# Performance work log

Hardware: AMD Instinct MI355X
Metric: run time of the kernel (lower is better)

Reference implementation:

```python
import jax, jax.numpy as jnp
import numpy as np

B, L, D = 16, 2048, 128
GROUP = 16
NG = L // GROUP  # number of groups per batch
ALPHA = 0.5


def setup_inputs() -> dict:
    key = jax.random.key(0)
    k0, k1, k2 = jax.random.split(key, 3)
    x = jax.random.normal(k0, (B, L, D), dtype=jnp.float32)
    # per-batch permutation = gather indices (each position used exactly once)
    group_tensor = jax.vmap(lambda k: jax.random.permutation(k, L))(
        jax.random.split(k1, B)).astype(jnp.int32)
    ctxlens = jnp.full((B,), L, dtype=jnp.int32)
    W = jax.random.normal(k2, (2 * D,), dtype=jnp.float32) * (1.0 / np.sqrt(D))
    norm_alpha = jnp.ones((2,), dtype=jnp.float32)
    norm_gamma = jnp.ones((2 * D,), dtype=jnp.float32)
    norm_beta = jnp.zeros((2 * D,), dtype=jnp.float32)
    return {"x": x, "group_tensor": group_tensor, "ctxlens": ctxlens, "W": W,
            "norm_alpha": norm_alpha, "norm_gamma": norm_gamma, "norm_beta": norm_beta}


def _leaky_relu(v):
    return jnp.where(v >= 0, v, 0.01 * v)


def _ncn_forward(x, group_tensor, ctxlens, W, norm_alpha, norm_gamma, norm_beta):
    Bd, Ld, Dd = x.shape
    ng = Ld // GROUP
    Wi, Wj = W[:Dd], W[Dd:]
    a1, a2 = norm_alpha[0], norm_alpha[1]
    g1, g2 = norm_gamma[:Dd], norm_gamma[Dd:]
    b1, b2 = norm_beta[:Dd], norm_beta[Dd:]

    # gather x by group indices -> [B, NG, GROUP, D]
    xg = jnp.take_along_axis(x, group_tensor[:, :, None].astype(jnp.int32), axis=1)
    xg = xg.reshape(Bd, ng, GROUP, Dd)

    def step(carry, j):
        xi, xa = carry  # each [B, NG, GROUP, D]
        xj = jax.lax.dynamic_slice_in_dim(xi, j, 1, axis=2)  # [B, NG, 1, D]
        sim = jnp.einsum('bgnd,d->bgn', xi, Wi) \
            + jnp.einsum('bgd,d->bg', xj[:, :, 0, :], Wj)[:, :, None]  # [B,NG,GROUP]
        T = ALPHA * xi + (1.0 - ALPHA) * sim[..., None] * xj
        T_norm = g1 * jnp.tanh(a1 * T) + b1
        Fv = _leaky_relu(T_norm)
        xa = xa + Fv                               # ya = xa + F
        xi = xi + g2 * jnp.tanh(a2 * xa) + b2      # yi = xi + norm2(ya)
        return (xi, xa), None

    (yi, ya), _ = jax.lax.scan(step, (xg, jnp.zeros_like(xg)), jnp.arange(GROUP))

    # kernel only processes/stores a group if its start offset < ctxlen
    valid = (jnp.arange(ng, dtype=jnp.int32) * GROUP)[None, :] < ctxlens[:, None]
    yi = jnp.where(valid[:, :, None, None], yi, 0.0).reshape(Bd, Ld, Dd)
    ya = jnp.where(valid[:, :, None, None], ya, 0.0).reshape(Bd, Ld, Dd)

    # scatter back to original positions
    bidx = jnp.arange(Bd)[:, None]
    yi_out = jnp.zeros_like(x).at[bidx, group_tensor].set(yi)
    ya_out = jnp.zeros_like(x).at[bidx, group_tensor].set(ya)
    return yi_out, ya_out


def reference(x, group_tensor, ctxlens, W, norm_alpha, norm_gamma, norm_beta):
    return _ncn_forward(x, group_tensor, ctxlens, W, norm_alpha, norm_gamma, norm_beta)
```

## Files before the change

kernel.cpp:

```cpp
#include <hip/hip_runtime.h>

#define B_ 16
#define L_ 2048
#define D_ 128
#define GROUP_ 16
#define NG_ (L_ / GROUP_)

__device__ __forceinline__ float tanh_fast(float v) {
    float e = __expf(2.0f * v);
    return 1.0f - 2.0f * __builtin_amdgcn_rcpf(e + 1.0f);
}

__global__ __launch_bounds__(256, 4) void ncn_kernel(
    const float* __restrict__ x,
    const int*   __restrict__ gt,
    const int*   __restrict__ ctxlens,
    const float* __restrict__ W,
    const float* __restrict__ nalpha,
    const float* __restrict__ ngamma,
    const float* __restrict__ nbeta,
    float* __restrict__ out)
{
    const int blk = blockIdx.x;
    const int b   = blk >> 7;
    const int g   = blk & (NG_ - 1);
    const int tid = threadIdx.x;
    const int row = tid >> 4;
    const int rl  = tid & 15;
    const int d0  = rl << 3;

    __shared__ float s_xj[D_];
    __shared__ float s_sjW;

    const float a1 = nalpha[0];
    const float a2 = nalpha[1];

    float Wi[8], Wj[8], g1v[8], b1v[8], g2v[8], b2v[8];
    *(float4*)&Wi[0]  = *(const float4*)(W + d0);
    *(float4*)&Wi[4]  = *(const float4*)(W + d0 + 4);
    *(float4*)&Wj[0]  = *(const float4*)(W + D_ + d0);
    *(float4*)&Wj[4]  = *(const float4*)(W + D_ + d0 + 4);
    *(float4*)&g1v[0] = *(const float4*)(ngamma + d0);
    *(float4*)&g1v[4] = *(const float4*)(ngamma + d0 + 4);
    *(float4*)&g2v[0] = *(const float4*)(ngamma + D_ + d0);
    *(float4*)&g2v[4] = *(const float4*)(ngamma + D_ + d0 + 4);
    *(float4*)&b1v[0] = *(const float4*)(nbeta + d0);
    *(float4*)&b1v[4] = *(const float4*)(nbeta + d0 + 4);
    *(float4*)&b2v[0] = *(const float4*)(nbeta + D_ + d0);
    *(float4*)&b2v[4] = *(const float4*)(nbeta + D_ + d0 + 4);

    const int l   = g * GROUP_ + row;
    const int tok = gt[b * L_ + l];
    const float* xp = x + ((size_t)(b * L_ + tok)) * D_ + d0;

    float xi[8], xa[8];
    *(float4*)&xi[0] = *(const float4*)xp;
    *(float4*)&xi[4] = *(const float4*)(xp + 4);
#pragma unroll
    for (int k = 0; k < 8; ++k) xa[k] = 0.0f;

    for (int j = 0; j < GROUP_; ++j) {
        if (row == j) {
            *(float4*)&s_xj[d0]     = *(float4*)&xi[0];
            *(float4*)&s_xj[d0 + 4] = *(float4*)&xi[4];
            float p = 0.0f;
#pragma unroll
            for (int k = 0; k < 8; ++k) p = fmaf(xi[k], Wj[k], p);
            p += __shfl_xor(p, 1);
            p += __shfl_xor(p, 2);
            p += __shfl_xor(p, 4);
            p += __shfl_xor(p, 8);
            if (rl == 0) s_sjW = p;
        }
        __syncthreads();

        float p = 0.0f;
#pragma unroll
        for (int k = 0; k < 8; ++k) p = fmaf(xi[k], Wi[k], p);
        p += __shfl_xor(p, 1);
        p += __shfl_xor(p, 2);
        p += __shfl_xor(p, 4);
        p += __shfl_xor(p, 8);
        const float sim = p + s_sjW;
        const float s2  = 0.5f * sim;

        float xjv[8];
        *(float4*)&xjv[0] = *(const float4*)&s_xj[d0];
        *(float4*)&xjv[4] = *(const float4*)&s_xj[d0 + 4];

#pragma unroll
        for (int k = 0; k < 8; ++k) {
            float T  = fmaf(0.5f, xi[k], s2 * xjv[k]);
            float t1 = tanh_fast(a1 * T);
            float tn = fmaf(g1v[k], t1, b1v[k]);
            float Fv = (tn >= 0.0f) ? tn : 0.01f * tn;
            xa[k] += Fv;
            float t2 = tanh_fast(a2 * xa[k]);
            xi[k] += fmaf(g2v[k], t2, b2v[k]);
        }
        __syncthreads();
    }

    const bool valid = (g * GROUP_) < ctxlens[b];
    if (!valid) {
#pragma unroll
        for (int k = 0; k < 8; ++k) { xi[k] = 0.0f; xa[k] = 0.0f; }
    }

    float* o1 = out + ((size_t)(b * L_ + tok)) * D_ + d0;
    float* o2 = o1 + (size_t)B_ * L_ * D_;
    *(float4*)o1       = *(float4*)&xi[0];
    *(float4*)(o1 + 4) = *(float4*)&xi[4];
    *(float4*)o2       = *(float4*)&xa[0];
    *(float4*)(o2 + 4) = *(float4*)&xa[4];
}

extern "C" void kernel_launch(void* const* d_in, const int* in_sizes, int n_in,
                              void* d_out, int out_size, void* d_ws, size_t ws_size,
                              hipStream_t stream) {
    const float* x  = (const float*)d_in[0];
    const int*   gt = (const int*)d_in[1];
    const int*   cl = (const int*)d_in[2];
    const float* W  = (const float*)d_in[3];
    const float* na = (const float*)d_in[4];
    const float* ng = (const float*)d_in[5];
    const float* nb = (const float*)d_in[6];
    float* out = (float*)d_out;

    ncn_kernel<<<B_ * NG_, 256, 0, stream>>>(x, gt, cl, W, na, ng, nb, out);
}
```

Measured before the change: 128.2 us.

## Double-buffer xj in shared memory and fold tanh affine into sigmoid form

Pivot rows are now written into a two-slot shared buffer right after each update, which cuts the block-wide barriers per step from two to one. The separate Wj reduction by the pivot row is dropped: each thread adds xj·Wj into its own dot product, so only one shuffle reduction runs per step. The tanh-then-affine is rewritten as a single exp/rcp sigmoid with gamma and beta pre-folded, and leaky ReLU becomes an fmax. Inline asm pins the parameter registers, which may raise register pressure.

```diff
diff --git a/kernel.cpp b/kernel.cpp
--- a/kernel.cpp
+++ b/kernel.cpp
@@ -5,11 +5,6 @@
 #define D_ 128
 #define GROUP_ 16
 #define NG_ (L_ / GROUP_)
-
-__device__ __forceinline__ float tanh_fast(float v) {
-    float e = __expf(2.0f * v);
-    return 1.0f - 2.0f * __builtin_amdgcn_rcpf(e + 1.0f);
-}
 
 __global__ __launch_bounds__(256, 4) void ncn_kernel(
     const float* __restrict__ x,
@@ -29,25 +24,45 @@
     const int rl  = tid & 15;
     const int d0  = rl << 3;
 
-    __shared__ float s_xj[D_];
-    __shared__ float s_sjW;
+    __shared__ float s_xj[2][D_];
 
     const float a1 = nalpha[0];
     const float a2 = nalpha[1];
+    const float m1 = -2.0f * a1;
+    const float m2 = -2.0f * a2;
 
-    float Wi[8], Wj[8], g1v[8], b1v[8], g2v[8], b2v[8];
-    *(float4*)&Wi[0]  = *(const float4*)(W + d0);
-    *(float4*)&Wi[4]  = *(const float4*)(W + d0 + 4);
-    *(float4*)&Wj[0]  = *(const float4*)(W + D_ + d0);
-    *(float4*)&Wj[4]  = *(const float4*)(W + D_ + d0 + 4);
-    *(float4*)&g1v[0] = *(const float4*)(ngamma + d0);
-    *(float4*)&g1v[4] = *(const float4*)(ngamma + d0 + 4);
-    *(float4*)&g2v[0] = *(const float4*)(ngamma + D_ + d0);
-    *(float4*)&g2v[4] = *(const float4*)(ngamma + D_ + d0 + 4);
-    *(float4*)&b1v[0] = *(const float4*)(nbeta + d0);
-    *(float4*)&b1v[4] = *(const float4*)(nbeta + d0 + 4);
-    *(float4*)&b2v[0] = *(const float4*)(nbeta + D_ + d0);
-    *(float4*)&b2v[4] = *(const float4*)(nbeta + D_ + d0 + 4);
+    float Wi[8], Wj[8], G1[8], B1[8], G2[8], B2[8];
+    {
+        float g1r[8], b1r[8], g2r[8], b2r[8];
+        *(float4*)&Wi[0]  = *(const float4*)(W + d0);
+        *(float4*)&Wi[4]  = *(const float4*)(W + d0 + 4);
+        *(float4*)&Wj[0]  = *(const float4*)(W + D_ + d0);
+        *(float4*)&Wj[4]  = *(const float4*)(W + D_ + d0 + 4);
+        *(float4*)&g1r[0] = *(const float4*)(ngamma + d0);
+        *(float4*)&g1r[4] = *(const float4*)(ngamma + d0 + 4);
+        *(float4*)&g2r[0] = *(const float4*)(ngamma + D_ + d0);
+        *(float4*)&g2r[4] = *(const float4*)(ngamma + D_ + d0 + 4);
+        *(float4*)&b1r[0] = *(const float4*)(nbeta + d0);
+        *(float4*)&b1r[4] = *(const float4*)(nbeta + d0 + 4);
+        *(float4*)&b2r[0] = *(const float4*)(nbeta + D_ + d0);
+        *(float4*)&b2r[4] = *(const float4*)(nbeta + D_ + d0 + 4);
+#pragma unroll
+        for (int k = 0; k < 8; ++k) {
+            G1[k] = 2.0f * g1r[k];
+            B1[k] = b1r[k] - g1r[k];
+            G2[k] = 2.0f * g2r[k];
+            B2[k] = b2r[k] - g2r[k];
+        }
+    }
+#pragma unroll
+    for (int k = 0; k < 8; ++k) {
+        asm volatile("" : "+v"(Wi[k]));
+        asm volatile("" : "+v"(Wj[k]));
+        asm volatile("" : "+v"(G1[k]));
+        asm volatile("" : "+v"(B1[k]));
+        asm volatile("" : "+v"(G2[k]));
+        asm volatile("" : "+v"(B2[k]));
+    }
 
     const int l   = g * GROUP_ + row;
     const int tok = gt[b * L_ + l];
@@ -59,44 +74,46 @@
 #pragma unroll
     for (int k = 0; k < 8; ++k) xa[k] = 0.0f;
 
+    if (row == 0) {
+        *(float4*)&s_xj[0][d0]     = *(float4*)&xi[0];
+        *(float4*)&s_xj[0][d0 + 4] = *(float4*)&xi[4];
+    }
+    __syncthreads();
+
     for (int j = 0; j < GROUP_; ++j) {
-        if (row == j) {
-            *(float4*)&s_xj[d0]     = *(float4*)&xi[0];
-            *(float4*)&s_xj[d0 + 4] = *(float4*)&xi[4];
-            float p = 0.0f;
-#pragma unroll
-            for (int k = 0; k < 8; ++k) p = fmaf(xi[k], Wj[k], p);
-            p += __shfl_xor(p, 1);
-            p += __shfl_xor(p, 2);
-            p += __shfl_xor(p, 4);
-            p += __shfl_xor(p, 8);
-            if (rl == 0) s_sjW = p;
-        }
-        __syncthreads();
-
-        float p = 0.0f;
-#pragma unroll
-        for (int k = 0; k < 8; ++k) p = fmaf(xi[k], Wi[k], p);
-        p += __shfl_xor(p, 1);
-        p += __shfl_xor(p, 2);
-        p += __shfl_xor(p, 4);
-        p += __shfl_xor(p, 8);
-        const float sim = p + s_sjW;
-        const float s2  = 0.5f * sim;
+        const int p = j & 1;
 
         float xjv[8];
-        *(float4*)&xjv[0] = *(const float4*)&s_xj[d0];
-        *(float4*)&xjv[4] = *(const float4*)&s_xj[d0 + 4];
+        *(float4*)&xjv[0] = *(const float4*)&s_xj[p][d0];
+        *(float4*)&xjv[4] = *(const float4*)&s_xj[p][d0 + 4];
+
+        float s = 0.0f;
+#pragma unroll
+        for (int k = 0; k < 8; ++k) s = fmaf(xi[k], Wi[k], s);
+#pragma unroll
+        for (int k = 0; k < 8; ++k) s = fmaf(xjv[k], Wj[k], s);
+        s += __shfl_xor(s, 1);
+        s += __shfl_xor(s, 2);
+        s += __shfl_xor(s, 4);
+        s += __shfl_xor(s, 8);
+        const float s2 = 0.5f * s;
 
 #pragma unroll
         for (int k = 0; k < 8; ++k) {
             float T  = fmaf(0.5f, xi[k], s2 * xjv[k]);
-            float t1 = tanh_fast(a1 * T);
-            float tn = fmaf(g1v[k], t1, b1v[k]);
-            float Fv = (tn >= 0.0f) ? tn : 0.01f * tn;
+            float e1 = __expf(m1 * T);
+            float r1 = __builtin_amdgcn_rcpf(1.0f + e1);
+            float tn = fmaf(G1[k], r1, B1[k]);
+            float Fv = fmaxf(tn, 0.01f * tn);
             xa[k] += Fv;
-            float t2 = tanh_fast(a2 * xa[k]);
-            xi[k] += fmaf(g2v[k], t2, b2v[k]);
+            float e2 = __expf(m2 * xa[k]);
+            float r2 = __builtin_amdgcn_rcpf(1.0f + e2);
+            xi[k] += fmaf(G2[k], r2, B2[k]);
+        }
+
+        if (j + 1 < GROUP_ && row == j + 1) {
+            *(float4*)&s_xj[p ^ 1][d0]     = *(float4*)&xi[0];
+            *(float4*)&s_xj[p ^ 1][d0 + 4] = *(float4*)&xi[4];
         }
         __syncthreads();
     }
```

New measurement: 123.5 us. 1.04x faster.
